# Kernel tuning notes

Hardware: AMD Instinct MI355X
Metric: run time of the kernel (lower is better)

Reference implementation:

```python
import jax, jax.numpy as jnp
import numpy as np
import math

B, S, H, NH = 4, 2048, 1024, 16
HD = H // NH  # head dim 64


def setup_inputs() -> dict:
    key = jax.random.key(0)
    ks = jax.random.split(key, 10)
    sc = 1.0 / math.sqrt(H)
    return {
        "x_q": jax.random.normal(ks[0], (B, S, H), jnp.float32),
        "x_k": jax.random.normal(ks[1], (B, S, H), jnp.float32),
        "x_v": jax.random.normal(ks[2], (B, S, H), jnp.float32),
        "att_mask": jnp.zeros((B, 1, 1, S), jnp.float32),
        "W_q": jax.random.normal(ks[3], (H, H), jnp.float32) * sc,
        "b_q": jnp.zeros((H,), jnp.float32),
        "W_k": jax.random.normal(ks[4], (H, H), jnp.float32) * sc,
        "b_k": jnp.zeros((H,), jnp.float32),
        "W_v": jax.random.normal(ks[5], (H, H), jnp.float32) * sc,
        "b_v": jnp.zeros((H,), jnp.float32),
    }


def reference(x_q, x_k, x_v, att_mask, W_q, b_q, W_k, b_k, W_v, b_v):
    # torch Linear: y = x @ W.T + b
    q = x_q @ W_q.T + b_q  # [B,S,H]
    k = x_k @ W_k.T + b_k
    v = x_v @ W_v.T + b_v
    q = q.reshape(B, S, NH, HD).transpose(0, 2, 1, 3)  # [B,NH,S,HD]
    k = k.reshape(B, S, NH, HD).transpose(0, 2, 1, 3)
    v = v.reshape(B, S, NH, HD).transpose(0, 2, 1, 3)
    scores = jnp.einsum('bhqd,bhkd->bhqk', q, k) / jnp.sqrt(jnp.float32(HD)) + att_mask
    probs = jax.nn.softmax(scores, axis=-1)
    ctx = jnp.einsum('bhqk,bhkd->bhqd', probs, v)  # [B,NH,S,HD]
    return ctx.transpose(0, 2, 1, 3).reshape(B, S, H)
```

## Files before the change

kernel.cpp:

```cpp
#include <hip/hip_runtime.h>

#define B_  4
#define S_  2048
#define H_  1024
#define NH_ 16
#define HD_ 64
#define MROWS (B_ * S_)
#define LOG2E 1.44269504f
#define MFIX  20.0f

typedef __attribute__((ext_vector_type(8))) short bf16x8;
typedef __attribute__((ext_vector_type(4))) float f32x4;
typedef unsigned short u16;
typedef unsigned int   u32;

__device__ __forceinline__ u16 f2bf(float f) {
  u32 u = __builtin_bit_cast(u32, f);
  u += 0x7fffu + ((u >> 16) & 1u);
  return (u16)(u >> 16);
}

__device__ __forceinline__ u32 cvtpk(float lo, float hi) {
  u32 r;
  asm("v_cvt_pk_bf16_f32 %0, %1, %2" : "=v"(r) : "v"(lo), "v"(hi));
  return r;
}

__device__ __forceinline__ float exp2_hw(float x) {
  float r;
  asm("v_exp_f32 %0, %1" : "=v"(r) : "v"(x));
  return r;
}
#define EXP2(x) exp2_hw(x)

typedef const __attribute__((address_space(1))) unsigned int cgu32;
typedef __attribute__((address_space(3))) unsigned int lsu32;
__device__ __forceinline__ void gload16(const void* g, void* l) {
  __builtin_amdgcn_global_load_lds((cgu32*)g, (lsu32*)l, 16, 0, 0);
}

__global__ __launch_bounds__(256) void cvt_x_k(const float* __restrict__ s0,
                                               const float* __restrict__ s1,
                                               const float* __restrict__ s2,
                                               u16* __restrict__ dst,
                                               size_t zstride) {
  int z = blockIdx.y;
  const float* src = (z == 0) ? s0 : (z == 1) ? s1 : s2;
  u16* d = dst + (size_t)z * zstride;
  size_t i = ((size_t)blockIdx.x * 256 + threadIdx.x) * 8;
  float4 f0 = *(const float4*)(src + i);
  float4 f1 = *(const float4*)(src + i + 4);
  uint4 o;
  o.x = cvtpk(f0.x, f0.y); o.y = cvtpk(f0.z, f0.w);
  o.z = cvtpk(f1.x, f1.y); o.w = cvtpk(f1.z, f1.w);
  *(uint4*)(d + i) = o;
}

#define BM 128
#define BN 128
#define BK 64

__global__ __launch_bounds__(256) void qkv_gemm_k(
    const u16* __restrict__ Xb, const u16* __restrict__ Wb,
    const float* __restrict__ bq, const float* __restrict__ bk,
    const float* __restrict__ bv, u16* __restrict__ qkv, int zsel) {
  int bid = blockIdx.x;
  int z, rr;
  if (zsel < 0) {
    int v = (bid & 7) * 192 + (bid >> 3);
    z = v >> 9; rr = v & 511;
  } else {
    z = zsel; rr = (bid & 7) * 64 + (bid >> 3);
  }
  int m0 = (rr >> 3) * BM, n0 = (rr & 7) * BN;

  const u16* X = (zsel < 0) ? Xb + (size_t)z * ((size_t)MROWS * H_) : Xb;
  const float* bias = (z == 0) ? bq : (z == 1) ? bk : bv;
  const u16*   W    = Wb + (size_t)z * (H_ * H_);
  u16*         out  = qkv + (size_t)z * (size_t)(B_ * NH_ * S_ * HD_);
  const float oscale = (z == 0) ? 0.125f * LOG2E : 1.0f;

  __shared__ u16 Al[2][BM * BK];
  __shared__ u16 Bl[2][BN * BK];

  int tid = threadIdx.x;
  int w = tid >> 6, l = tid & 63;
  int wm = (w >> 1) * 64, wn = (w & 1) * 64;

  f32x4 acc[4][4];
#pragma unroll
  for (int i = 0; i < 4; ++i)
#pragma unroll
    for (int j = 0; j < 4; ++j) acc[i][j] = (f32x4){0.f, 0.f, 0.f, 0.f};

  int lr = l >> 3, lg = (l & 7) ^ lr;

  auto issueB = [&](int bf, int k0) {
#pragma unroll
    for (int i = 0; i < 4; ++i) {
      int row = w * 32 + i * 8;
      gload16(W + (size_t)(n0 + row + lr) * H_ + k0 + lg * 8, &Bl[bf][row * BK]);
    }
  };
  auto issueA = [&](int bf, int k0) {
#pragma unroll
    for (int i = 0; i < 4; ++i) {
      int row = w * 32 + i * 8;
      gload16(X + (size_t)(m0 + row + lr) * H_ + k0 + lg * 8, &Al[bf][row * BK]);
    }
  };

  issueA(0, 0);
  issueB(0, 0);
  __syncthreads();

  int buf = 0;
  const int NT = H_ / BK;
  for (int t = 0; t < NT; ++t) {
    if (t + 1 < NT) {
      issueA(buf ^ 1, (t + 1) * BK);
      issueB(buf ^ 1, (t + 1) * BK);
    }
    __builtin_amdgcn_s_setprio(1);
#pragma unroll
    for (int kc = 0; kc < 2; ++kc) {
      int col = kc * 32 + (l >> 4) * 8;
      bf16x8 a[4], b[4];
#pragma unroll
      for (int mf = 0; mf < 4; ++mf) {
        int row = wm + mf * 16 + (l & 15);
        a[mf] = *(const bf16x8*)&Al[buf][row * BK + (col ^ ((row & 7) << 3))];
      }
#pragma unroll
      for (int nf = 0; nf < 4; ++nf) {
        int row = wn + nf * 16 + (l & 15);
        b[nf] = *(const bf16x8*)&Bl[buf][row * BK + (col ^ ((row & 7) << 3))];
      }
#pragma unroll
      for (int mf = 0; mf < 4; ++mf)
#pragma unroll
        for (int nf = 0; nf < 4; ++nf)
          acc[mf][nf] = __builtin_amdgcn_mfma_f32_16x16x32_bf16(
              a[mf], b[nf], acc[mf][nf], 0, 0, 0);
    }
    __builtin_amdgcn_s_setprio(0);
    __syncthreads();
    buf ^= 1;
  }

#pragma unroll
  for (int nf = 0; nf < 4; ++nf) {
    int n = n0 + wn + nf * 16 + (l & 15);
    float bv_ = bias[n];
    int h = n >> 6, d = n & 63;
    if (z == 2) {
#pragma unroll
      for (int mf = 0; mf < 4; ++mf) {
        int m = m0 + wm + mf * 16 + (l >> 4) * 4;
        int bb = m >> 11, ss = m & 2047;
        int u = ss & 63, w31 = u & 31;
        int pos = (u & 32) | (((w31 & 15) >> 2) << 3) | (w31 & 3) |
                  (((w31 >> 4) & 1) << 2);
        int ssp = (ss & ~63) | pos;
        uint2 pk;
        pk.x = cvtpk(acc[mf][nf][0] + bv_, acc[mf][nf][1] + bv_);
        pk.y = cvtpk(acc[mf][nf][2] + bv_, acc[mf][nf][3] + bv_);
        *(uint2*)&out[((size_t)(bb * NH_ + h) * HD_ + d) * S_ + ssp] = pk;
      }
    } else {
#pragma unroll
      for (int mf = 0; mf < 4; ++mf) {
#pragma unroll
        for (int r = 0; r < 4; ++r) {
          int m = m0 + wm + mf * 16 + (l >> 4) * 4 + r;
          int bb = m >> 11, ss = m & 2047;
          float vv = (acc[mf][nf][r] + bv_) * oscale;
          out[(size_t)((bb * NH_ + h) * S_ + ss) * HD_ + d] = f2bf(vv);
        }
      }
    }
  }
}

__global__ __launch_bounds__(256) void qkv_gemm_fb_k(
    const float* __restrict__ xq, const float* __restrict__ xk,
    const float* __restrict__ xv, const u16* __restrict__ Wb,
    const float* __restrict__ bq, const float* __restrict__ bk,
    const float* __restrict__ bv, u16* __restrict__ qkv) {
  int bid = blockIdx.x;
  int v = (bid & 7) * 192 + (bid >> 3);
  int z = v >> 9;
  int rr = v & 511;
  int m0 = (rr >> 3) * BM, n0 = (rr & 7) * BN;

  const float* X    = (z == 0) ? xq : (z == 1) ? xk : xv;
  const float* bias = (z == 0) ? bq : (z == 1) ? bk : bv;
  const u16*   W    = Wb + (size_t)z * (H_ * H_);
  u16*         out  = qkv + (size_t)z * (size_t)(B_ * NH_ * S_ * HD_);
  const float oscale = (z == 0) ? 0.125f * LOG2E : 1.0f;

  __shared__ u16 Al[2][BM * BK];
  __shared__ u16 Bl[2][BN * BK];

  int tid = threadIdx.x;
  int w = tid >> 6, l = tid & 63;
  int wm = (w >> 1) * 64, wn = (w & 1) * 64;

  f32x4 acc[4][4];
#pragma unroll
  for (int i = 0; i < 4; ++i)
#pragma unroll
    for (int j = 0; j < 4; ++j) acc[i][j] = (f32x4){0.f, 0.f, 0.f, 0.f};

  int lr = l >> 3, lg = (l & 7) ^ lr;

  float4 ar[4][2];
  auto issueB = [&](int bf, int k0) {
#pragma unroll
    for (int i = 0; i < 4; ++i) {
      int row = w * 32 + i * 8;
      gload16(W + (size_t)(n0 + row + lr) * H_ + k0 + lg * 8, &Bl[bf][row * BK]);
    }
  };
  auto loadA = [&](int k0) {
#pragma unroll
    for (int it = 0; it < 4; ++it) {
      int slot = it * 256 + tid;
      int r = slot >> 3, c8 = (slot & 7) * 8;
      const float* s = X + (size_t)(m0 + r) * H_ + k0 + c8;
      ar[it][0] = *(const float4*)s;
      ar[it][1] = *(const float4*)(s + 4);
    }
  };
  auto writeA = [&](int bf) {
#pragma unroll
    for (int it = 0; it < 4; ++it) {
      int slot = it * 256 + tid;
      int r = slot >> 3, c8 = (slot & 7) * 8;
      int lidx = r * BK + (c8 ^ ((r & 7) << 3));
      uint4 o;
      o.x = cvtpk(ar[it][0].x, ar[it][0].y);
      o.y = cvtpk(ar[it][0].z, ar[it][0].w);
      o.z = cvtpk(ar[it][1].x, ar[it][1].y);
      o.w = cvtpk(ar[it][1].z, ar[it][1].w);
      *(uint4*)&Al[bf][lidx] = o;
    }
  };

  issueB(0, 0);
  loadA(0);
  writeA(0);
  __syncthreads();

  int buf = 0;
  const int NT = H_ / BK;
  for (int t = 0; t < NT; ++t) {
    if (t + 1 < NT) {
      issueB(buf ^ 1, (t + 1) * BK);
      loadA((t + 1) * BK);
    }
    __builtin_amdgcn_s_setprio(1);
#pragma unroll
    for (int kc = 0; kc < 2; ++kc) {
      int col = kc * 32 + (l >> 4) * 8;
      bf16x8 a[4], b[4];
#pragma unroll
      for (int mf = 0; mf < 4; ++mf) {
        int row = wm + mf * 16 + (l & 15);
        a[mf] = *(const bf16x8*)&Al[buf][row * BK + (col ^ ((row & 7) << 3))];
      }
#pragma unroll
      for (int nf = 0; nf < 4; ++nf) {
        int row = wn + nf * 16 + (l & 15);
        b[nf] = *(const bf16x8*)&Bl[buf][row * BK + (col ^ ((row & 7) << 3))];
      }
#pragma unroll
      for (int mf = 0; mf < 4; ++mf)
#pragma unroll
        for (int nf = 0; nf < 4; ++nf)
          acc[mf][nf] = __builtin_amdgcn_mfma_f32_16x16x32_bf16(
              a[mf], b[nf], acc[mf][nf], 0, 0, 0);
    }
    __builtin_amdgcn_s_setprio(0);
    if (t + 1 < NT) writeA(buf ^ 1);
    __syncthreads();
    buf ^= 1;
  }

#pragma unroll
  for (int nf = 0; nf < 4; ++nf) {
    int n = n0 + wn + nf * 16 + (l & 15);
    float bv_ = bias[n];
    int h = n >> 6, d = n & 63;
    if (z == 2) {
#pragma unroll
      for (int mf = 0; mf < 4; ++mf) {
        int m = m0 + wm + mf * 16 + (l >> 4) * 4;
        int bb = m >> 11, ss = m & 2047;
        int u = ss & 63, w31 = u & 31;
        int pos = (u & 32) | (((w31 & 15) >> 2) << 3) | (w31 & 3) |
                  (((w31 >> 4) & 1) << 2);
        int ssp = (ss & ~63) | pos;
        uint2 pk;
        pk.x = cvtpk(acc[mf][nf][0] + bv_, acc[mf][nf][1] + bv_);
        pk.y = cvtpk(acc[mf][nf][2] + bv_, acc[mf][nf][3] + bv_);
        *(uint2*)&out[((size_t)(bb * NH_ + h) * HD_ + d) * S_ + ssp] = pk;
      }
    } else {
#pragma unroll
      for (int mf = 0; mf < 4; ++mf) {
#pragma unroll
        for (int r = 0; r < 4; ++r) {
          int m = m0 + wm + mf * 16 + (l >> 4) * 4 + r;
          int bb = m >> 11, ss = m & 2047;
          float vv = (acc[mf][nf][r] + bv_) * oscale;
          out[(size_t)((bb * NH_ + h) * S_ + ss) * HD_ + d] = f2bf(vv);
        }
      }
    }
  }
}

__global__ __launch_bounds__(256, 2) void attn_k(const u16* __restrict__ qkv,
                                                 const float* __restrict__ mask,
                                                 float* __restrict__ out) {
  const u16* Qg  = qkv;
  const u16* Kg  = qkv + (size_t)(B_ * NH_ * S_ * HD_);
  const u16* Vtg = qkv + (size_t)2 * (B_ * NH_ * S_ * HD_);

  int tid = threadIdx.x, w = tid >> 6, l = tid & 63;
  int bh = blockIdx.x;
  int b = bh >> 4, h = bh & 15;
  int q0 = blockIdx.y * 256;
  int qw = q0 + w * 64;

  __shared__ u16 Kl[3][64 * 64];
  __shared__ u16 Vl[3][64 * 64];
  __shared__ float Mla[S_];

  const u16* kbase = Kg + (size_t)bh * S_ * HD_;
  const u16* vbase = Vtg + (size_t)bh * HD_ * S_;
  const float* maskb = mask + b * S_;
  int lr = l >> 3, lg = (l & 7) ^ lr;

  {
    float4 m4 = *(const float4*)(maskb + tid * 4);
    m4.x = m4.x * LOG2E - MFIX; m4.y = m4.y * LOG2E - MFIX;
    m4.z = m4.z * LOG2E - MFIX; m4.w = m4.w * LOG2E - MFIX;
    ((float4*)Mla)[tid] = m4;
    float4 m5 = *(const float4*)(maskb + (tid + 256) * 4);
    m5.x = m5.x * LOG2E - MFIX; m5.y = m5.y * LOG2E - MFIX;
    m5.z = m5.z * LOG2E - MFIX; m5.w = m5.w * LOG2E - MFIX;
    ((float4*)Mla)[tid + 256] = m5;
  }

  bf16x8 qf0[4], qf1[4];
#pragma unroll
  for (int qs = 0; qs < 4; ++qs) {
    const u16* qr = Qg + ((size_t)bh * S_ + qw + qs * 16 + (l & 15)) * HD_ +
                    (l >> 4) * 8;
    qf0[qs] = *(const bf16x8*)qr;
    qf1[qs] = *(const bf16x8*)(qr + 32);
  }

  float lsum[4] = {0.f, 0.f, 0.f, 0.f};
  f32x4 o[4][4];
#pragma unroll
  for (int qs = 0; qs < 4; ++qs)
#pragma unroll
    for (int i = 0; i < 4; ++i) o[qs][i] = (f32x4){0.f, 0.f, 0.f, 0.f};

  auto stage = [&](int bf, int kv0) {
    int rb = w * 16;
    gload16(kbase + (size_t)(kv0 + rb + lr) * HD_ + lg * 8, &Kl[bf][rb * 64]);
    gload16(kbase + (size_t)(kv0 + rb + 8 + lr) * HD_ + lg * 8,
            &Kl[bf][(rb + 8) * 64]);
    gload16(vbase + (size_t)(rb + lr) * S_ + kv0 + lg * 8, &Vl[bf][rb * 64]);
    gload16(vbase + (size_t)(rb + 8 + lr) * S_ + kv0 + lg * 8,
            &Vl[bf][(rb + 8) * 64]);
  };

  __syncthreads();
  stage(0, 0);
  stage(1, 64);

  const int NT = S_ / 64;
  int cur = 0;
  for (int t = 0; t < NT; ++t) {
    if (t < NT - 1) asm volatile("s_waitcnt vmcnt(4)" ::: "memory");
    else            asm volatile("s_waitcnt vmcnt(0)" ::: "memory");
    __builtin_amdgcn_s_barrier();
    __builtin_amdgcn_sched_barrier(0);

    if (t + 2 < NT) {
      int nxt = cur + 2; if (nxt >= 3) nxt -= 3;
      stage(nxt, (t + 2) * 64);
    }

    f32x4 sc[4][4];
    int colq = (l >> 4) * 8;
    __builtin_amdgcn_s_setprio(1);
#pragma unroll
    for (int f = 0; f < 4; ++f) {
      int row = f * 16 + (l & 15);
      int swz = (row & 7) << 3;
      bf16x8 k0 = *(const bf16x8*)&Kl[cur][row * 64 + (colq ^ swz)];
      bf16x8 k1 = *(const bf16x8*)&Kl[cur][row * 64 + ((colq + 32) ^ swz)];
#pragma unroll
      for (int qs = 0; qs < 4; ++qs) {
        f32x4 z = (f32x4){0.f, 0.f, 0.f, 0.f};
        z = __builtin_amdgcn_mfma_f32_16x16x32_bf16(k0, qf0[qs], z, 0, 0, 0);
        z = __builtin_amdgcn_mfma_f32_16x16x32_bf16(k1, qf1[qs], z, 0, 0, 0);
        sc[qs][f] = z;
      }
    }
    __builtin_amdgcn_s_setprio(0);

    u32 pk[4][8];
#pragma unroll
    for (int f = 0; f < 4; ++f) {
      float4 mk = *(const float4*)&Mla[t * 64 + f * 16 + (l >> 4) * 4];
#pragma unroll
      for (int qs = 0; qs < 4; ++qs) {
        float p0 = EXP2(sc[qs][f][0] + mk.x), p1 = EXP2(sc[qs][f][1] + mk.y);
        float p2 = EXP2(sc[qs][f][2] + mk.z), p3 = EXP2(sc[qs][f][3] + mk.w);
        lsum[qs] += (p0 + p1) + (p2 + p3);
        pk[qs][f * 2]     = cvtpk(p0, p1);
        pk[qs][f * 2 + 1] = cvtpk(p2, p3);
      }
    }

    __builtin_amdgcn_s_setprio(1);
#pragma unroll
    for (int kc = 0; kc < 2; ++kc) {
      int kvc = kc * 32 + (l >> 4) * 8;
      bf16x8 pfr[4];
#pragma unroll
      for (int qs = 0; qs < 4; ++qs) {
        uint4 tu;
        tu.x = pk[qs][4 * kc + 0]; tu.y = pk[qs][4 * kc + 1];
        tu.z = pk[qs][4 * kc + 2]; tu.w = pk[qs][4 * kc + 3];
        pfr[qs] = __builtin_bit_cast(bf16x8, tu);
      }
#pragma unroll
      for (int df = 0; df < 4; ++df) {
        int row = df * 16 + (l & 15);
        bf16x8 vf = *(const bf16x8*)&Vl[cur][row * 64 + (kvc ^ ((row & 7) << 3))];
#pragma unroll
        for (int qs = 0; qs < 4; ++qs)
          o[qs][df] = __builtin_amdgcn_mfma_f32_16x16x32_bf16(vf, pfr[qs],
                                                             o[qs][df], 0, 0, 0);
      }
    }
    __builtin_amdgcn_s_setprio(0);

    cur = (cur == 2) ? 0 : cur + 1;
  }

#pragma unroll
  for (int qs = 0; qs < 4; ++qs) {
    lsum[qs] += __shfl_xor(lsum[qs], 16);
    lsum[qs] += __shfl_xor(lsum[qs], 32);
    float inv = 1.0f / lsum[qs];
    float* ob = out + ((size_t)b * S_ + qw + qs * 16 + (l & 15)) * H_ + h * HD_;
#pragma unroll
    for (int df = 0; df < 4; ++df) {
      int d0 = df * 16 + (l >> 4) * 4;
      float4 r;
      r.x = o[qs][df][0] * inv; r.y = o[qs][df][1] * inv;
      r.z = o[qs][df][2] * inv; r.w = o[qs][df][3] * inv;
      *(float4*)(ob + d0) = r;
    }
  }
}

extern "C" void kernel_launch(void* const* d_in, const int* in_sizes, int n_in,
                              void* d_out, int out_size, void* d_ws, size_t ws_size,
                              hipStream_t stream) {
  const float* xq = (const float*)d_in[0];
  const float* xk = (const float*)d_in[1];
  const float* xv = (const float*)d_in[2];
  const float* mask = (const float*)d_in[3];
  const float* Wq = (const float*)d_in[4];
  const float* bq = (const float*)d_in[5];
  const float* Wk = (const float*)d_in[6];
  const float* bk = (const float*)d_in[7];
  const float* Wv = (const float*)d_in[8];
  const float* bv = (const float*)d_in[9];
  float* outp = (float*)d_out;

  const size_t WbE  = (size_t)3 * H_ * H_;
  const size_t QKVE = (size_t)3 * B_ * NH_ * S_ * HD_;
  const size_t XE1  = (size_t)MROWS * H_;

  u16* Wb  = (u16*)d_ws;
  u16* qkv = Wb + WbE;
  u16* Xb  = qkv + QKVE;

  const size_t need_full = (WbE + QKVE + 3 * XE1) * 2;
  const size_t need_seq  = (WbE + QKVE + XE1) * 2;

  cvt_x_k<<<dim3(H_ * H_ / 2048, 3), 256, 0, stream>>>(Wq, Wk, Wv, Wb,
                                                       (size_t)H_ * H_);

  if (ws_size >= need_full) {
    cvt_x_k<<<dim3(XE1 / 2048, 3), 256, 0, stream>>>(xq, xk, xv, Xb, XE1);
    qkv_gemm_k<<<dim3(3 * (MROWS / BM) * (H_ / BN)), 256, 0, stream>>>(
        Xb, Wb, bq, bk, bv, qkv, -1);
  } else if (ws_size >= need_seq) {
    const float* xs[3] = {xq, xk, xv};
    for (int z = 0; z < 3; ++z) {
      cvt_x_k<<<dim3(XE1 / 2048, 1), 256, 0, stream>>>(xs[z], xs[z], xs[z],
                                                       Xb, 0);
      qkv_gemm_k<<<dim3((MROWS / BM) * (H_ / BN)), 256, 0, stream>>>(
          Xb, Wb, bq, bk, bv, qkv, z);
    }
  } else {
    qkv_gemm_fb_k<<<dim3(3 * (MROWS / BM) * (H_ / BN)), 256, 0, stream>>>(
        xq, xk, xv, Wb, bq, bk, bv, qkv);
  }

  attn_k<<<dim3(B_ * NH_, S_ / 256), 256, 0, stream>>>(qkv, mask, outp);
}
```

Baseline: 168.2 us.

## Enlarge QKV GEMM tiles to 256x256 with 8 waves and finer-grained barriers

```diff
diff --git a/kernel.cpp b/kernel.cpp
--- a/kernel.cpp
+++ b/kernel.cpp
@@ -56,23 +56,23 @@
   *(uint4*)(d + i) = o;
 }
 
-#define BM 128
-#define BN 128
-#define BK 64
-
-__global__ __launch_bounds__(256) void qkv_gemm_k(
+#define GBM 256
+#define GBN 256
+#define GBK 64
+
+__global__ __launch_bounds__(512, 2) void qkv_gemm8_k(
     const u16* __restrict__ Xb, const u16* __restrict__ Wb,
     const float* __restrict__ bq, const float* __restrict__ bk,
     const float* __restrict__ bv, u16* __restrict__ qkv, int zsel) {
   int bid = blockIdx.x;
   int z, rr;
   if (zsel < 0) {
-    int v = (bid & 7) * 192 + (bid >> 3);
-    z = v >> 9; rr = v & 511;
+    int v = (bid & 7) * 48 + (bid >> 3);
+    z = v >> 7; rr = v & 127;
   } else {
-    z = zsel; rr = (bid & 7) * 64 + (bid >> 3);
-  }
-  int m0 = (rr >> 3) * BM, n0 = (rr & 7) * BN;
+    z = zsel; rr = bid;
+  }
+  int m0 = (rr >> 2) * GBM, n0 = (rr & 3) * GBN;
 
   const u16* X = (zsel < 0) ? Xb + (size_t)z * ((size_t)MROWS * H_) : Xb;
   const float* bias = (z == 0) ? bq : (z == 1) ? bk : bv;
@@ -80,72 +80,83 @@
   u16*         out  = qkv + (size_t)z * (size_t)(B_ * NH_ * S_ * HD_);
   const float oscale = (z == 0) ? 0.125f * LOG2E : 1.0f;
 
-  __shared__ u16 Al[2][BM * BK];
-  __shared__ u16 Bl[2][BN * BK];
+  __shared__ u16 Al[2][GBM * GBK];
+  __shared__ u16 Bl[2][GBN * GBK];
 
   int tid = threadIdx.x;
   int w = tid >> 6, l = tid & 63;
-  int wm = (w >> 1) * 64, wn = (w & 1) * 64;
-
-  f32x4 acc[4][4];
-#pragma unroll
-  for (int i = 0; i < 4; ++i)
+  int wm = (w >> 2) * 128, wn = (w & 3) * 64;
+
+  f32x4 acc[8][4];
+#pragma unroll
+  for (int i = 0; i < 8; ++i)
 #pragma unroll
     for (int j = 0; j < 4; ++j) acc[i][j] = (f32x4){0.f, 0.f, 0.f, 0.f};
 
   int lr = l >> 3, lg = (l & 7) ^ lr;
 
-  auto issueB = [&](int bf, int k0) {
-#pragma unroll
-    for (int i = 0; i < 4; ++i) {
-      int row = w * 32 + i * 8;
-      gload16(W + (size_t)(n0 + row + lr) * H_ + k0 + lg * 8, &Bl[bf][row * BK]);
+  auto stageTile = [&](int kt) {
+    int slot = kt & 1;
+    int k0 = kt * GBK;
+#pragma unroll
+    for (int h = 0; h < 4; ++h) {
+#pragma unroll
+      for (int c = 0; c < 2; ++c) {
+        int row = (h & 1) * 128 + w * 16 + c * 8;
+        if (h < 2)
+          gload16(X + (size_t)(m0 + row + lr) * H_ + k0 + lg * 8,
+                  &Al[slot][row * GBK]);
+        else
+          gload16(W + (size_t)(n0 + row + lr) * H_ + k0 + lg * 8,
+                  &Bl[slot][row * GBK]);
+      }
     }
   };
-  auto issueA = [&](int bf, int k0) {
-#pragma unroll
-    for (int i = 0; i < 4; ++i) {
-      int row = w * 32 + i * 8;
-      gload16(X + (size_t)(m0 + row + lr) * H_ + k0 + lg * 8, &Al[bf][row * BK]);
-    }
-  };
-
-  issueA(0, 0);
-  issueB(0, 0);
-  __syncthreads();
-
-  int buf = 0;
-  const int NT = H_ / BK;
+
+  stageTile(0);
+  asm volatile("s_waitcnt vmcnt(0)" ::: "memory");
+  __builtin_amdgcn_s_barrier();
+
+  const int NT = H_ / GBK;
+  bf16x8 a[8];
   for (int t = 0; t < NT; ++t) {
-    if (t + 1 < NT) {
-      issueA(buf ^ 1, (t + 1) * BK);
-      issueB(buf ^ 1, (t + 1) * BK);
-    }
-    __builtin_amdgcn_s_setprio(1);
-#pragma unroll
-    for (int kc = 0; kc < 2; ++kc) {
+    int slot = t & 1;
+#pragma unroll
+    for (int q = 0; q < 4; ++q) {
+      if (q == 0) {
+        if (t + 1 < NT) {
+          stageTile(t + 1);
+          asm volatile("s_waitcnt vmcnt(8)" ::: "memory");
+        } else {
+          asm volatile("s_waitcnt vmcnt(0)" ::: "memory");
+        }
+        __builtin_amdgcn_s_barrier();
+      }
+      int kc = q >> 1;
       int col = kc * 32 + (l >> 4) * 8;
-      bf16x8 a[4], b[4];
-#pragma unroll
-      for (int mf = 0; mf < 4; ++mf) {
-        int row = wm + mf * 16 + (l & 15);
-        a[mf] = *(const bf16x8*)&Al[buf][row * BK + (col ^ ((row & 7) << 3))];
-      }
-#pragma unroll
-      for (int nf = 0; nf < 4; ++nf) {
-        int row = wn + nf * 16 + (l & 15);
-        b[nf] = *(const bf16x8*)&Bl[buf][row * BK + (col ^ ((row & 7) << 3))];
-      }
-#pragma unroll
-      for (int mf = 0; mf < 4; ++mf)
-#pragma unroll
-        for (int nf = 0; nf < 4; ++nf)
-          acc[mf][nf] = __builtin_amdgcn_mfma_f32_16x16x32_bf16(
-              a[mf], b[nf], acc[mf][nf], 0, 0, 0);
-    }
-    __builtin_amdgcn_s_setprio(0);
-    __syncthreads();
-    buf ^= 1;
+      if ((q & 1) == 0) {
+#pragma unroll
+        for (int mf = 0; mf < 8; ++mf) {
+          int row = wm + mf * 16 + (l & 15);
+          a[mf] = *(const bf16x8*)&Al[slot][row * GBK + (col ^ ((row & 7) << 3))];
+        }
+      }
+      int nf0 = (q & 1) * 2;
+      int row0 = wn + nf0 * 16 + (l & 15);
+      int row1 = row0 + 16;
+      bf16x8 b0 = *(const bf16x8*)&Bl[slot][row0 * GBK + (col ^ ((row0 & 7) << 3))];
+      bf16x8 b1 = *(const bf16x8*)&Bl[slot][row1 * GBK + (col ^ ((row1 & 7) << 3))];
+      __builtin_amdgcn_s_setprio(1);
+#pragma unroll
+      for (int mf = 0; mf < 8; ++mf) {
+        acc[mf][nf0]     = __builtin_amdgcn_mfma_f32_16x16x32_bf16(
+            a[mf], b0, acc[mf][nf0], 0, 0, 0);
+        acc[mf][nf0 + 1] = __builtin_amdgcn_mfma_f32_16x16x32_bf16(
+            a[mf], b1, acc[mf][nf0 + 1], 0, 0, 0);
+      }
+      __builtin_amdgcn_s_setprio(0);
+      __builtin_amdgcn_s_barrier();
+    }
   }
 
 #pragma unroll
@@ -155,7 +166,7 @@
     int h = n >> 6, d = n & 63;
     if (z == 2) {
 #pragma unroll
-      for (int mf = 0; mf < 4; ++mf) {
+      for (int mf = 0; mf < 8; ++mf) {
         int m = m0 + wm + mf * 16 + (l >> 4) * 4;
         int bb = m >> 11, ss = m & 2047;
         int u = ss & 63, w31 = u & 31;
@@ -169,7 +180,7 @@
       }
     } else {
 #pragma unroll
-      for (int mf = 0; mf < 4; ++mf) {
+      for (int mf = 0; mf < 8; ++mf) {
 #pragma unroll
         for (int r = 0; r < 4; ++r) {
           int m = m0 + wm + mf * 16 + (l >> 4) * 4 + r;
@@ -181,6 +192,10 @@
     }
   }
 }
+
+#define BM 128
+#define BN 128
+#define BK 64
 
 __global__ __launch_bounds__(256) void qkv_gemm_fb_k(
     const float* __restrict__ xq, const float* __restrict__ xk,
@@ -505,14 +520,14 @@
 
   if (ws_size >= need_full) {
     cvt_x_k<<<dim3(XE1 / 2048, 3), 256, 0, stream>>>(xq, xk, xv, Xb, XE1);
-    qkv_gemm_k<<<dim3(3 * (MROWS / BM) * (H_ / BN)), 256, 0, stream>>>(
+    qkv_gemm8_k<<<dim3(3 * (MROWS / GBM) * (H_ / GBN)), 512, 0, stream>>>(
         Xb, Wb, bq, bk, bv, qkv, -1);
   } else if (ws_size >= need_seq) {
     const float* xs[3] = {xq, xk, xv};
     for (int z = 0; z < 3; ++z) {
       cvt_x_k<<<dim3(XE1 / 2048, 1), 256, 0, stream>>>(xs[z], xs[z], xs[z],
                                                        Xb, 0);
-      qkv_gemm_k<<<dim3((MROWS / BM) * (H_ / BN)), 256, 0, stream>>>(
+      qkv_gemm8_k<<<dim3((MROWS / GBM) * (H_ / GBN)), 512, 0, stream>>>(
           Xb, Wb, bq, bk, bv, qkv, z);
     }
   } else {
```

New measurement: 188.2 us. 11.9% more time.
